# Optimization experiments

Measured on AMD Instinct MI355X. Metric: run time of the kernel, lower is better.

Reference implementation:

```python
import jax, jax.numpy as jnp
import numpy as np

L_LAYERS = 6
D_MODEL = 1024
N_HEAD = 16
D_K = D_MODEL // N_HEAD
D_FF = 4096
EPS = 1e-5


def _mk(key, shape, scale=0.02):
    return jax.random.normal(key, shape, dtype=jnp.float32) * scale


def setup_inputs() -> dict:
    key = jax.random.key(0)
    ks = jax.random.split(key, 18)
    B, S = 4, 1024
    L, D, F = L_LAYERS, D_MODEL, D_FF
    return {
        "x": jax.random.normal(ks[0], (B, S, D), dtype=jnp.float32),
        # weights stored [in, out] so y = x @ W + b
        "Wq": _mk(ks[1], (L, D, D)), "bq": jnp.zeros((L, D), jnp.float32),
        "Wk": _mk(ks[2], (L, D, D)), "bk": jnp.zeros((L, D), jnp.float32),
        "Wv": _mk(ks[3], (L, D, D)), "bv": jnp.zeros((L, D), jnp.float32),
        "Wo": _mk(ks[4], (L, D, D)), "bo": jnp.zeros((L, D), jnp.float32),
        "W1": _mk(ks[5], (L, D, F)), "b1": jnp.zeros((L, F), jnp.float32),
        "W2": _mk(ks[6], (L, F, D)), "b2": jnp.zeros((L, D), jnp.float32),
        "g1": jnp.ones((L, D), jnp.float32), "be1": jnp.zeros((L, D), jnp.float32),
        "g2": jnp.ones((L, D), jnp.float32), "be2": jnp.zeros((L, D), jnp.float32),
    }


def _layernorm(x, g, b):
    mu = jnp.mean(x, axis=-1, keepdims=True)
    var = jnp.mean(jnp.square(x - mu), axis=-1, keepdims=True)
    return (x - mu) * jax.lax.rsqrt(var + EPS) * g + b


def _encoder(x, params):
    B, S, D = x.shape
    scale = 1.0 / jnp.sqrt(jnp.asarray(D_K, x.dtype))

    def layer(x, p):
        Wq, bq, Wk, bk, Wv, bv, Wo, bo, W1, b1, W2, b2, g1, be1, g2, be2 = p
        q = (x @ Wq + bq).reshape(B, S, N_HEAD, D_K).transpose(0, 2, 1, 3)
        k = (x @ Wk + bk).reshape(B, S, N_HEAD, D_K).transpose(0, 2, 1, 3)
        v = (x @ Wv + bv).reshape(B, S, N_HEAD, D_K).transpose(0, 2, 1, 3)
        scores = jnp.einsum('bhqd,bhkd->bhqk', q, k) * scale  # [B,H,S,S]
        attn = jax.nn.softmax(scores, axis=-1)
        o = jnp.einsum('bhqk,bhkd->bhqd', attn, v)
        o = o.transpose(0, 2, 1, 3).reshape(B, S, N_HEAD * D_K)
        sa = o @ Wo + bo
        x = _layernorm(x + sa, g1, be1)  # post-LN (norm_first=False)
        h = jax.nn.relu(x @ W1 + b1)
        ff = h @ W2 + b2
        x = _layernorm(x + ff, g2, be2)
        return x, None

    x, _ = jax.lax.scan(layer, x, params)
    return x


def reference(x, Wq, bq, Wk, bk, Wv, bv, Wo, bo, W1, b1, W2, b2, g1, be1, g2, be2):
    params = (Wq, bq, Wk, bk, Wv, bv, Wo, bo, W1, b1, W2, b2, g1, be1, g2, be2)
    return _encoder(x, params)
```

## Files before the change

### kernel.cpp

```cpp
#include <hip/hip_runtime.h>


#define D_MODEL 1024
#define N_HEAD 16
#define D_K 64
#define D_FF 4096
#define SEQ 1024
#define BATCH 4
#define ROWS (BATCH * SEQ)
#define LAYERS 6

typedef __attribute__((ext_vector_type(4))) float floatx4;
typedef __attribute__((ext_vector_type(8))) short shortx8;
typedef __attribute__((ext_vector_type(8))) unsigned short ushortx8;
typedef __attribute__((ext_vector_type(4))) unsigned short ushortx4;

__device__ __forceinline__ unsigned short f32_to_bf16(float f) {
  unsigned int u = __float_as_uint(f);
  u = u + 0x7FFFu + ((u >> 16) & 1u);
  return (unsigned short)(u >> 16);
}
__device__ __forceinline__ float bf16_to_f32(unsigned short s) {
  return __uint_as_float(((unsigned int)s) << 16);
}
__device__ __forceinline__ void split8(const float* f, shortx8& hi, shortx8& lo) {
#pragma unroll
  for (int j = 0; j < 8; ++j) {
    unsigned short hb = f32_to_bf16(f[j]);
    hi[j] = (short)hb;
    lo[j] = (short)f32_to_bf16(f[j] - bf16_to_f32(hb));
  }
}

__device__ __forceinline__ void wtrans_body(
    const float* __restrict__ W, unsigned short* __restrict__ th,
    unsigned short* __restrict__ tl, int K, int N, int k0, int n0) {
  __shared__ float tile[32][33];
  const int tid = threadIdx.x;
  {
    const int r = tid >> 3;
    const int c4 = (tid & 7) * 4;
    float4 v = *(const float4*)&W[(size_t)(k0 + r) * N + n0 + c4];
    tile[r][c4 + 0] = v.x; tile[r][c4 + 1] = v.y;
    tile[r][c4 + 2] = v.z; tile[r][c4 + 3] = v.w;
  }
  __syncthreads();
  {
    const int n = tid >> 3;
    const int k4 = (tid & 7) * 4;
    ushortx4 h, l;
#pragma unroll
    for (int j = 0; j < 4; ++j) {
      float f = tile[k4 + j][n];
      unsigned short hb = f32_to_bf16(f);
      h[j] = hb;
      l[j] = f32_to_bf16(f - bf16_to_f32(hb));
    }
    *(ushortx4*)&th[(size_t)(n0 + n) * K + k0 + k4] = h;
    *(ushortx4*)&tl[(size_t)(n0 + n) * K + k0 + k4] = l;
  }
}

__global__ __launch_bounds__(256) void wtrans_kernel(
    const float* __restrict__ W, unsigned short* __restrict__ th,
    unsigned short* __restrict__ tl, int K, int N) {
  wtrans_body(W, th, tl, K, N, blockIdx.x * 32, blockIdx.y * 32);
}

__global__ __launch_bounds__(256) void wtrans_qkvo_kernel(
    const float* __restrict__ Wq, const float* __restrict__ Wk,
    const float* __restrict__ Wv, const float* __restrict__ Wo,
    unsigned short* __restrict__ qh, unsigned short* __restrict__ ql,
    unsigned short* __restrict__ kh, unsigned short* __restrict__ kl,
    unsigned short* __restrict__ vh, unsigned short* __restrict__ vl,
    unsigned short* __restrict__ oh, unsigned short* __restrict__ ol) {
  const float* W;
  unsigned short *th, *tl;
  switch (blockIdx.z) {
    case 0: W = Wq; th = qh; tl = ql; break;
    case 1: W = Wk; th = kh; tl = kl; break;
    case 2: W = Wv; th = vh; tl = vl; break;
    default: W = Wo; th = oh; tl = ol; break;
  }
  wtrans_body(W, th, tl, D_MODEL, D_MODEL, blockIdx.x * 32, blockIdx.y * 32);
}

__global__ __launch_bounds__(256) void split_kernel(
    const float* __restrict__ in, unsigned short* __restrict__ hi,
    unsigned short* __restrict__ lo, int n4) {
  int i = blockIdx.x * 256 + threadIdx.x;
  if (i >= n4) return;
  float4 v = ((const float4*)in)[i];
  float f[4] = {v.x, v.y, v.z, v.w};
  ushortx4 h, l;
#pragma unroll
  for (int j = 0; j < 4; ++j) {
    unsigned short hb = f32_to_bf16(f[j]);
    h[j] = hb;
    l[j] = f32_to_bf16(f[j] - bf16_to_f32(hb));
  }
  ((ushortx4*)hi)[i] = h;
  ((ushortx4*)lo)[i] = l;
}

#define GBM 128
#define GBN 64
#define GBK 32
#define LDSP 40

template <int RELU, int OUTBF16>
__global__ __launch_bounds__(256) void gemm_mfma_kernel(
    const unsigned short* __restrict__ Ahi, const unsigned short* __restrict__ Alo,
    const unsigned short* __restrict__ Bhi, const unsigned short* __restrict__ Blo,
    const float* __restrict__ bias, float* __restrict__ C,
    unsigned short* __restrict__ Chi, unsigned short* __restrict__ Clo,
    int M, int N, int K) {
  __shared__ unsigned short As[2][GBM][LDSP];
  __shared__ unsigned short Bs[2][GBN][LDSP];

  const int tid = threadIdx.x;
  const int wave = tid >> 6;
  const int lane = tid & 63;
  const int row0 = blockIdx.y * GBM;
  const int col0 = blockIdx.x * GBN;
  const int wr = (wave >> 1) * 64;
  const int wc = (wave & 1) * 32;
  const int lr = lane & 15;
  const int lk = (lane >> 4) * 8;

  const unsigned short* const ap[2] = {Ahi, Alo};
  const unsigned short* const bp[2] = {Bhi, Blo};

  const int sr = tid >> 2;
  const int sc = (tid & 3) * 8;

  floatx4 acc[4][2];
#pragma unroll
  for (int i = 0; i < 4; ++i)
#pragma unroll
    for (int j = 0; j < 2; ++j) acc[i][j] = (floatx4)0.f;

  for (int k0 = 0; k0 < K; k0 += GBK) {
    ushortx8 a_st[2][2], b_st[2];
#pragma unroll
    for (int arr = 0; arr < 2; ++arr) {
#pragma unroll
      for (int half = 0; half < 2; ++half)
        a_st[arr][half] = *(const ushortx8*)(ap[arr] +
            (size_t)(row0 + sr + half * 64) * K + k0 + sc);
      b_st[arr] = *(const ushortx8*)(bp[arr] + (size_t)(col0 + sr) * K + k0 + sc);
    }
    __syncthreads();
#pragma unroll
    for (int arr = 0; arr < 2; ++arr) {
#pragma unroll
      for (int half = 0; half < 2; ++half)
        *(ushortx8*)&As[arr][sr + half * 64][sc] = a_st[arr][half];
      *(ushortx8*)&Bs[arr][sr][sc] = b_st[arr];
    }
    __syncthreads();

    shortx8 ah[4], al[4], bh[2], bl[2];
#pragma unroll
    for (int mi = 0; mi < 4; ++mi) {
      ah[mi] = *(const shortx8*)&As[0][wr + mi * 16 + lr][lk];
      al[mi] = *(const shortx8*)&As[1][wr + mi * 16 + lr][lk];
    }
#pragma unroll
    for (int ni = 0; ni < 2; ++ni) {
      bh[ni] = *(const shortx8*)&Bs[0][wc + ni * 16 + lr][lk];
      bl[ni] = *(const shortx8*)&Bs[1][wc + ni * 16 + lr][lk];
    }
#pragma unroll
    for (int mi = 0; mi < 4; ++mi)
#pragma unroll
      for (int ni = 0; ni < 2; ++ni) {
        acc[mi][ni] = __builtin_amdgcn_mfma_f32_16x16x32_bf16(
            ah[mi], bh[ni], acc[mi][ni], 0, 0, 0);
        acc[mi][ni] = __builtin_amdgcn_mfma_f32_16x16x32_bf16(
            al[mi], bh[ni], acc[mi][ni], 0, 0, 0);
        acc[mi][ni] = __builtin_amdgcn_mfma_f32_16x16x32_bf16(
            ah[mi], bl[ni], acc[mi][ni], 0, 0, 0);
      }
  }

#pragma unroll
  for (int ni = 0; ni < 2; ++ni) {
    const int col = col0 + wc + ni * 16 + lr;
    const float bv = bias[col];
#pragma unroll
    for (int mi = 0; mi < 4; ++mi) {
      const int rowb = row0 + wr + mi * 16 + (lane >> 4) * 4;
#pragma unroll
      for (int j = 0; j < 4; ++j) {
        float val = acc[mi][ni][j] + bv;
        if (RELU) val = fmaxf(val, 0.f);
        const size_t idx = (size_t)(rowb + j) * N + col;
        if (OUTBF16) {
          unsigned short hb = f32_to_bf16(val);
          Chi[idx] = hb;
          Clo[idx] = f32_to_bf16(val - bf16_to_f32(hb));
        } else {
          C[idx] = val;
        }
      }
    }
  }
}

#define QB 64
#define KB 64

__global__ __launch_bounds__(256) void attn_mfma_kernel(
    const float* __restrict__ q, const float* __restrict__ k,
    const float* __restrict__ v, unsigned short* __restrict__ ohi,
    unsigned short* __restrict__ olo) {
  __shared__ unsigned short Kh[64 * 64], Kl[64 * 64];
  __shared__ unsigned short Vh[64 * 64], Vl[64 * 64];
  __shared__ unsigned short Ph[4][16 * 64], Pl[4][16 * 64];

  const int tid = threadIdx.x;
  const int w = tid >> 6;
  const int l = tid & 63;
  const int lr = l & 15;
  const int lg = l >> 4;
  const int qb = blockIdx.x;
  const int bh = blockIdx.y;
  const int b = bh >> 4;
  const int h = bh & 15;
  const size_t base = (size_t)b * SEQ * D_MODEL + (size_t)h * D_K;

  shortx8 Qh[2], Ql[2];
  {
    const float* qrow = q + base + (size_t)(qb * QB + w * 16 + lr) * D_MODEL;
#pragma unroll
    for (int s = 0; s < 2; ++s) {
      float f[8];
      *(float4*)&f[0] = *(const float4*)&qrow[s * 32 + lg * 8];
      *(float4*)&f[4] = *(const float4*)&qrow[s * 32 + lg * 8 + 4];
#pragma unroll
      for (int j = 0; j < 8; ++j) f[j] *= 0.125f;
      split8(f, Qh[s], Ql[s]);
    }
  }

  floatx4 acc_o[4];
#pragma unroll
  for (int i = 0; i < 4; ++i) acc_o[i] = (floatx4)0.f;
  float m_run[4] = {-1e30f, -1e30f, -1e30f, -1e30f};
  float l_run[4] = {0.f, 0.f, 0.f, 0.f};

  for (int kt = 0; kt < SEQ / KB; ++kt) {
    __syncthreads();
#pragma unroll
    for (int it = 0; it < 2; ++it) {
      const int idx = tid + it * 256;
      const int kk = idx >> 3, dblk = idx & 7;
      const float* kr = k + base + (size_t)(kt * KB + kk) * D_MODEL + dblk * 8;
      float f[8];
      *(float4*)&f[0] = *(const float4*)kr;
      *(float4*)&f[4] = *(const float4*)(kr + 4);
      shortx8 hi, lo;
      split8(f, hi, lo);
      const int a = kk * 64 + ((dblk ^ (kk & 7)) * 8);
      *(shortx8*)&Kh[a] = hi;
      *(shortx8*)&Kl[a] = lo;
    }
#pragma unroll
    for (int it = 0; it < 2; ++it) {
      const int g = w + it * 4;
      const int d = l;
      float f[8];
#pragma unroll
      for (int j = 0; j < 8; ++j)
        f[j] = v[base + (size_t)(kt * KB + g * 8 + j) * D_MODEL + d];
      shortx8 hi, lo;
      split8(f, hi, lo);
      const int a = d * 64 + ((g ^ (d & 7)) * 8);
      *(shortx8*)&Vh[a] = hi;
      *(shortx8*)&Vl[a] = lo;
    }
    __syncthreads();

    floatx4 sfr[4];
#pragma unroll
    for (int f = 0; f < 4; ++f) {
      floatx4 acc = (floatx4)0.f;
      const int kk = f * 16 + lr;
#pragma unroll
      for (int s = 0; s < 2; ++s) {
        const int a = kk * 64 + (((s * 4 + lg) ^ (kk & 7)) * 8);
        shortx8 kbh = *(const shortx8*)&Kh[a];
        shortx8 kbl = *(const shortx8*)&Kl[a];
        acc = __builtin_amdgcn_mfma_f32_16x16x32_bf16(Qh[s], kbh, acc, 0, 0, 0);
        acc = __builtin_amdgcn_mfma_f32_16x16x32_bf16(Ql[s], kbh, acc, 0, 0, 0);
        acc = __builtin_amdgcn_mfma_f32_16x16x32_bf16(Qh[s], kbl, acc, 0, 0, 0);
      }
      sfr[f] = acc;
    }

    float corr[4];
#pragma unroll
    for (int j = 0; j < 4; ++j) {
      float tm = fmaxf(fmaxf(sfr[0][j], sfr[1][j]), fmaxf(sfr[2][j], sfr[3][j]));
      tm = fmaxf(tm, __shfl_xor(tm, 1));
      tm = fmaxf(tm, __shfl_xor(tm, 2));
      tm = fmaxf(tm, __shfl_xor(tm, 4));
      tm = fmaxf(tm, __shfl_xor(tm, 8));
      const float mn = fmaxf(m_run[j], tm);
      corr[j] = __expf(m_run[j] - mn);
      m_run[j] = mn;
      float ps = 0.f;
#pragma unroll
      for (int f = 0; f < 4; ++f) {
        float p = __expf(sfr[f][j] - mn);
        sfr[f][j] = p;
        ps += p;
      }
      ps += __shfl_xor(ps, 1);
      ps += __shfl_xor(ps, 2);
      ps += __shfl_xor(ps, 4);
      ps += __shfl_xor(ps, 8);
      l_run[j] = l_run[j] * corr[j] + ps;
#pragma unroll
      for (int nf = 0; nf < 4; ++nf) acc_o[nf][j] *= corr[j];
    }

    unsigned short* phw = &Ph[w][0];
    unsigned short* plw = &Pl[w][0];
#pragma unroll
    for (int f = 0; f < 4; ++f) {
      const int kk = f * 16 + lr;
      const int blk = kk >> 3;
      const int within = kk & 7;
#pragma unroll
      for (int j = 0; j < 4; ++j) {
        const int qr = lg * 4 + j;
        const float p = sfr[f][j];
        const unsigned short hb = f32_to_bf16(p);
        const int a = qr * 64 + ((blk ^ (qr & 7)) * 8) + within;
        phw[a] = hb;
        plw[a] = f32_to_bf16(p - bf16_to_f32(hb));
      }
    }

#pragma unroll
    for (int s2 = 0; s2 < 2; ++s2) {
      const int blk = (s2 * 4 + lg) ^ (lr & 7);
      shortx8 pah = *(const shortx8*)&Ph[w][lr * 64 + blk * 8];
      shortx8 pal = *(const shortx8*)&Pl[w][lr * 64 + blk * 8];
#pragma unroll
      for (int nf = 0; nf < 4; ++nf) {
        const int d = nf * 16 + lr;
        const int a = d * 64 + blk * 8;
        shortx8 vbh = *(const shortx8*)&Vh[a];
        shortx8 vbl = *(const shortx8*)&Vl[a];
        acc_o[nf] = __builtin_amdgcn_mfma_f32_16x16x32_bf16(pah, vbh, acc_o[nf], 0, 0, 0);
        acc_o[nf] = __builtin_amdgcn_mfma_f32_16x16x32_bf16(pal, vbh, acc_o[nf], 0, 0, 0);
        acc_o[nf] = __builtin_amdgcn_mfma_f32_16x16x32_bf16(pah, vbl, acc_o[nf], 0, 0, 0);
      }
    }
  }

  float inv[4];
#pragma unroll
  for (int j = 0; j < 4; ++j) inv[j] = 1.f / l_run[j];
#pragma unroll
  for (int nf = 0; nf < 4; ++nf) {
    const int d = nf * 16 + lr;
#pragma unroll
    for (int j = 0; j < 4; ++j) {
      const int qr = lg * 4 + j;
      const float val = acc_o[nf][j] * inv[j];
      const size_t idx = base + (size_t)(qb * QB + w * 16 + qr) * D_MODEL + d;
      const unsigned short hb = f32_to_bf16(val);
      ohi[idx] = hb;
      olo[idx] = f32_to_bf16(val - bf16_to_f32(hb));
    }
  }
}

__global__ __launch_bounds__(256) void add_ln_kernel(
    float* __restrict__ x, const float* __restrict__ t,
    const float* __restrict__ gamma, const float* __restrict__ beta,
    unsigned short* __restrict__ xh, unsigned short* __restrict__ xl) {
  const int row = blockIdx.x;
  const int tid = threadIdx.x;
  float* xrow = x + (size_t)row * D_MODEL;
  const float* trow = t + (size_t)row * D_MODEL;

  float4 xv = ((const float4*)xrow)[tid];
  float4 tv = ((const float4*)trow)[tid];
  float4 s;
  s.x = xv.x + tv.x; s.y = xv.y + tv.y;
  s.z = xv.z + tv.z; s.w = xv.w + tv.w;

  float sum = s.x + s.y + s.z + s.w;
  float sq = s.x * s.x + s.y * s.y + s.z * s.z + s.w * s.w;
#pragma unroll
  for (int off = 32; off > 0; off >>= 1) {
    sum += __shfl_down(sum, off);
    sq += __shfl_down(sq, off);
  }
  __shared__ float red[10];
  const int wave = tid >> 6;
  if ((tid & 63) == 0) { red[wave] = sum; red[wave + 4] = sq; }
  __syncthreads();
  if (tid == 0) {
    float S = red[0] + red[1] + red[2] + red[3];
    float Q = red[4] + red[5] + red[6] + red[7];
    float mu = S * (1.f / D_MODEL);
    float var = Q * (1.f / D_MODEL) - mu * mu;
    red[8] = mu;
    red[9] = rsqrtf(var + 1e-5f);
  }
  __syncthreads();
  const float mu = red[8], rstd = red[9];

  float4 gv = ((const float4*)gamma)[tid];
  float4 bv = ((const float4*)beta)[tid];
  float f[4];
  f[0] = (s.x - mu) * rstd * gv.x + bv.x;
  f[1] = (s.y - mu) * rstd * gv.y + bv.y;
  f[2] = (s.z - mu) * rstd * gv.z + bv.z;
  f[3] = (s.w - mu) * rstd * gv.w + bv.w;
  ((float4*)xrow)[tid] = make_float4(f[0], f[1], f[2], f[3]);

  ushortx4 h4, l4;
#pragma unroll
  for (int j = 0; j < 4; ++j) {
    unsigned short hb = f32_to_bf16(f[j]);
    h4[j] = hb;
    l4[j] = f32_to_bf16(f[j] - bf16_to_f32(hb));
  }
  const size_t o4 = (size_t)row * (D_MODEL / 4) + tid;
  ((ushortx4*)xh)[o4] = h4;
  ((ushortx4*)xl)[o4] = l4;
}

extern "C" void kernel_launch(void* const* d_in, const int* in_sizes, int n_in,
                              void* d_out, int out_size, void* d_ws,
                              size_t ws_size, hipStream_t stream) {
  const float* x  = (const float*)d_in[0];
  const float* Wq = (const float*)d_in[1];
  const float* bq = (const float*)d_in[2];
  const float* Wk = (const float*)d_in[3];
  const float* bk = (const float*)d_in[4];
  const float* Wv = (const float*)d_in[5];
  const float* bv = (const float*)d_in[6];
  const float* Wo = (const float*)d_in[7];
  const float* bo = (const float*)d_in[8];
  const float* W1 = (const float*)d_in[9];
  const float* b1 = (const float*)d_in[10];
  const float* W2 = (const float*)d_in[11];
  const float* b2 = (const float*)d_in[12];
  const float* g1 = (const float*)d_in[13];
  const float* be1 = (const float*)d_in[14];
  const float* g2 = (const float*)d_in[15];
  const float* be2 = (const float*)d_in[16];

  float* xb = (float*)d_out;
  char* ws = (char*)d_ws;
  const size_t MB = 1024ull * 1024ull;
  const size_t NTOK = (size_t)ROWS * D_MODEL;

  float* qf = (float*)(ws + 0 * MB);
  float* kf = (float*)(ws + 16 * MB);
  float* vf = (float*)(ws + 32 * MB);
  float* t0 = (float*)(ws + 64 * MB);
  unsigned short* xh = (unsigned short*)(ws + 80 * MB);
  unsigned short* xl = (unsigned short*)(ws + 88 * MB);
  unsigned short* oh = (unsigned short*)(ws + 96 * MB);
  unsigned short* ol = (unsigned short*)(ws + 104 * MB);
  unsigned short* hh = (unsigned short*)(ws + 0 * MB);
  unsigned short* hl = (unsigned short*)(ws + 32 * MB);
  unsigned short* wqh = (unsigned short*)(ws + 112 * MB);
  unsigned short* wql = (unsigned short*)(ws + 114 * MB);
  unsigned short* wkh = (unsigned short*)(ws + 116 * MB);
  unsigned short* wkl = (unsigned short*)(ws + 118 * MB);
  unsigned short* wvh = (unsigned short*)(ws + 120 * MB);
  unsigned short* wvl = (unsigned short*)(ws + 122 * MB);
  unsigned short* woh = (unsigned short*)(ws + 124 * MB);
  unsigned short* wol = (unsigned short*)(ws + 126 * MB);
  unsigned short* w1h = (unsigned short*)(ws + 128 * MB);
  unsigned short* w1l = (unsigned short*)(ws + 136 * MB);
  unsigned short* w2h = (unsigned short*)(ws + 144 * MB);
  unsigned short* w2l = (unsigned short*)(ws + 152 * MB);

  hipMemcpyAsync(xb, x, NTOK * sizeof(float), hipMemcpyDeviceToDevice, stream);

  const dim3 blk(256);
  const dim3 g_dd(D_MODEL / GBN, ROWS / GBM);
  const dim3 g_df(D_FF / GBN, ROWS / GBM);
  const dim3 attn_grid(SEQ / QB, BATCH * N_HEAD);
  const dim3 ln_grid(ROWS);
  const int n4tok = (int)(NTOK / 4);

  split_kernel<<<dim3((n4tok + 255) / 256), blk, 0, stream>>>(xb, xh, xl, n4tok);

  for (int l = 0; l < LAYERS; ++l) {
    const float* Wq_l = Wq + (size_t)l * D_MODEL * D_MODEL;
    const float* Wk_l = Wk + (size_t)l * D_MODEL * D_MODEL;
    const float* Wv_l = Wv + (size_t)l * D_MODEL * D_MODEL;
    const float* Wo_l = Wo + (size_t)l * D_MODEL * D_MODEL;
    const float* W1_l = W1 + (size_t)l * D_MODEL * D_FF;
    const float* W2_l = W2 + (size_t)l * D_FF * D_MODEL;
    const float* bq_l = bq + (size_t)l * D_MODEL;
    const float* bk_l = bk + (size_t)l * D_MODEL;
    const float* bv_l = bv + (size_t)l * D_MODEL;
    const float* bo_l = bo + (size_t)l * D_MODEL;
    const float* b1_l = b1 + (size_t)l * D_FF;
    const float* b2_l = b2 + (size_t)l * D_MODEL;
    const float* g1_l = g1 + (size_t)l * D_MODEL;
    const float* be1_l = be1 + (size_t)l * D_MODEL;
    const float* g2_l = g2 + (size_t)l * D_MODEL;
    const float* be2_l = be2 + (size_t)l * D_MODEL;

    wtrans_qkvo_kernel<<<dim3(32, 32, 4), blk, 0, stream>>>(
        Wq_l, Wk_l, Wv_l, Wo_l, wqh, wql, wkh, wkl, wvh, wvl, woh, wol);
    wtrans_kernel<<<dim3(32, 128), blk, 0, stream>>>(W1_l, w1h, w1l, D_MODEL, D_FF);
    wtrans_kernel<<<dim3(128, 32), blk, 0, stream>>>(W2_l, w2h, w2l, D_FF, D_MODEL);

    gemm_mfma_kernel<0, 0><<<g_dd, blk, 0, stream>>>(
        xh, xl, wqh, wql, bq_l, qf, nullptr, nullptr, ROWS, D_MODEL, D_MODEL);
    gemm_mfma_kernel<0, 0><<<g_dd, blk, 0, stream>>>(
        xh, xl, wkh, wkl, bk_l, kf, nullptr, nullptr, ROWS, D_MODEL, D_MODEL);
    gemm_mfma_kernel<0, 0><<<g_dd, blk, 0, stream>>>(
        xh, xl, wvh, wvl, bv_l, vf, nullptr, nullptr, ROWS, D_MODEL, D_MODEL);

    attn_mfma_kernel<<<attn_grid, blk, 0, stream>>>(qf, kf, vf, oh, ol);

    gemm_mfma_kernel<0, 0><<<g_dd, blk, 0, stream>>>(
        oh, ol, woh, wol, bo_l, t0, nullptr, nullptr, ROWS, D_MODEL, D_MODEL);
    add_ln_kernel<<<ln_grid, blk, 0, stream>>>(xb, t0, g1_l, be1_l, xh, xl);

    gemm_mfma_kernel<1, 1><<<g_df, blk, 0, stream>>>(
        xh, xl, w1h, w1l, b1_l, nullptr, hh, hl, ROWS, D_FF, D_MODEL);
    gemm_mfma_kernel<0, 0><<<g_dd, blk, 0, stream>>>(
        hh, hl, w2h, w2l, b2_l, t0, nullptr, nullptr, ROWS, D_MODEL, D_FF);
    add_ln_kernel<<<ln_grid, blk, 0, stream>>>(xb, t0, g2_l, be2_l, xh, xl);
  }
}
```

Measured before the change: 3.992 ms.

## Load GEMM tiles directly into LDS and swizzle workgroup order

Replaces the register-staged global-to-LDS copies in the split-bf16 MFMA GEMM with global_load_lds direct transfers into unpadded LDS tiles. It also remaps workgroup IDs with an 8-way swizzle to improve L2 locality between neighbouring blocks. This removes VGPR staging and ds_write instructions, but drops the LDS row padding, which may cause bank conflicts on the MFMA fragment reads. The swizzle assumes the workgroup count is divisible by 8.

```diff
diff --git a/kernel.cpp b/kernel.cpp
--- a/kernel.cpp
+++ b/kernel.cpp
@@ -14,6 +14,11 @@
 typedef __attribute__((ext_vector_type(8))) short shortx8;
 typedef __attribute__((ext_vector_type(8))) unsigned short ushortx8;
 typedef __attribute__((ext_vector_type(4))) unsigned short ushortx4;
+
+typedef const __attribute__((address_space(1))) unsigned int ga_u32;
+typedef __attribute__((address_space(3))) unsigned int lds_u32;
+#define GLD16(gp, lp) __builtin_amdgcn_global_load_lds( \
+    (ga_u32*)(gp), (lds_u32*)(lp), 16, 0, 0)
 
 __device__ __forceinline__ unsigned short f32_to_bf16(float f) {
   unsigned int u = __float_as_uint(f);
@@ -106,7 +111,6 @@
 #define GBM 128
 #define GBN 64
 #define GBK 32
-#define LDSP 40
 
 template <int RELU, int OUTBF16>
 __global__ __launch_bounds__(256) void gemm_mfma_kernel(
@@ -115,24 +119,39 @@
     const float* __restrict__ bias, float* __restrict__ C,
     unsigned short* __restrict__ Chi, unsigned short* __restrict__ Clo,
     int M, int N, int K) {
-  __shared__ unsigned short As[2][GBM][LDSP];
-  __shared__ unsigned short Bs[2][GBN][LDSP];
+  __shared__ unsigned short AsH[GBM * GBK];
+  __shared__ unsigned short AsL[GBM * GBK];
+  __shared__ unsigned short BsH[GBN * GBK];
+  __shared__ unsigned short BsL[GBN * GBK];
 
   const int tid = threadIdx.x;
   const int wave = tid >> 6;
   const int lane = tid & 63;
-  const int row0 = blockIdx.y * GBM;
-  const int col0 = blockIdx.x * GBN;
+
+  const int gx = gridDim.x;
+  const int nwg = gx * gridDim.y;
+  const int flat = blockIdx.y * gx + blockIdx.x;
+  const int swz = (flat & 7) * (nwg >> 3) + (flat >> 3);
+  const int row0 = (swz / gx) * GBM;
+  const int col0 = (swz % gx) * GBN;
+
   const int wr = (wave >> 1) * 64;
   const int wc = (wave & 1) * 32;
   const int lr = lane & 15;
   const int lk = (lane >> 4) * 8;
 
-  const unsigned short* const ap[2] = {Ahi, Alo};
-  const unsigned short* const bp[2] = {Bhi, Blo};
-
-  const int sr = tid >> 2;
-  const int sc = (tid & 3) * 8;
+  const int rl = lane >> 2;
+  const int ce = (lane & 3) * 8;
+
+  const size_t aoff0 = (size_t)(row0 + 32 * wave + rl) * K + ce;
+  const size_t aoff1 = aoff0 + (size_t)16 * K;
+  const size_t boff  = (size_t)(col0 + 16 * wave + rl) * K + ce;
+  unsigned short* const asd0 = AsH + (32 * wave) * GBK;
+  unsigned short* const asd1 = AsH + (32 * wave + 16) * GBK;
+  unsigned short* const ald0 = AsL + (32 * wave) * GBK;
+  unsigned short* const ald1 = AsL + (32 * wave + 16) * GBK;
+  unsigned short* const bsd  = BsH + (16 * wave) * GBK;
+  unsigned short* const bld  = BsL + (16 * wave) * GBK;
 
   floatx4 acc[4][2];
 #pragma unroll
@@ -141,35 +160,25 @@
     for (int j = 0; j < 2; ++j) acc[i][j] = (floatx4)0.f;
 
   for (int k0 = 0; k0 < K; k0 += GBK) {
-    ushortx8 a_st[2][2], b_st[2];
-#pragma unroll
-    for (int arr = 0; arr < 2; ++arr) {
-#pragma unroll
-      for (int half = 0; half < 2; ++half)
-        a_st[arr][half] = *(const ushortx8*)(ap[arr] +
-            (size_t)(row0 + sr + half * 64) * K + k0 + sc);
-      b_st[arr] = *(const ushortx8*)(bp[arr] + (size_t)(col0 + sr) * K + k0 + sc);
-    }
     __syncthreads();
-#pragma unroll
-    for (int arr = 0; arr < 2; ++arr) {
-#pragma unroll
-      for (int half = 0; half < 2; ++half)
-        *(ushortx8*)&As[arr][sr + half * 64][sc] = a_st[arr][half];
-      *(ushortx8*)&Bs[arr][sr][sc] = b_st[arr];
-    }
+    GLD16(Ahi + aoff0 + k0, asd0);
+    GLD16(Ahi + aoff1 + k0, asd1);
+    GLD16(Alo + aoff0 + k0, ald0);
+    GLD16(Alo + aoff1 + k0, ald1);
+    GLD16(Bhi + boff + k0, bsd);
+    GLD16(Blo + boff + k0, bld);
     __syncthreads();
 
     shortx8 ah[4], al[4], bh[2], bl[2];
 #pragma unroll
     for (int mi = 0; mi < 4; ++mi) {
-      ah[mi] = *(const shortx8*)&As[0][wr + mi * 16 + lr][lk];
-      al[mi] = *(const shortx8*)&As[1][wr + mi * 16 + lr][lk];
+      ah[mi] = *(const shortx8*)&AsH[(wr + mi * 16 + lr) * GBK + lk];
+      al[mi] = *(const shortx8*)&AsL[(wr + mi * 16 + lr) * GBK + lk];
     }
 #pragma unroll
     for (int ni = 0; ni < 2; ++ni) {
-      bh[ni] = *(const shortx8*)&Bs[0][wc + ni * 16 + lr][lk];
-      bl[ni] = *(const shortx8*)&Bs[1][wc + ni * 16 + lr][lk];
+      bh[ni] = *(const shortx8*)&BsH[(wc + ni * 16 + lr) * GBK + lk];
+      bl[ni] = *(const shortx8*)&BsL[(wc + ni * 16 + lr) * GBK + lk];
     }
 #pragma unroll
     for (int mi = 0; mi < 4; ++mi)
```

New measurement: 3.701 ms. 7.3% less time.
